# Kernel optimization log

Measured on AMD Instinct MI355X. Metric: run time of the kernel, lower is better.

The kernel has to match this reference:

```python
import jax, jax.numpy as jnp
import numpy as np

IMG = 1024.0          # input image size (square)
PRE_NMS_TOPK = 1000   # per level (test-time)
POST_NMS_TOPK = 1000
NMS_THRESH = 0.7
MIN_BOX_SIZE = 0.0
A = 3                 # anchors (aspect ratios) per location
SIZES = [32, 64, 128, 256, 512]
STRIDES = [4, 8, 16, 32, 64]
FEATS = [256, 128, 64, 32, 16]
RATIOS = [0.5, 1.0, 2.0]
B = 8


def _make_anchors():
    out = []
    for size, stride, f in zip(SIZES, STRIDES, FEATS):
        base = np.stack([np.array([-size * np.sqrt(r) / 2, -size / np.sqrt(r) / 2,
                                   size * np.sqrt(r) / 2, size / np.sqrt(r) / 2])
                         for r in RATIOS])  # [A,4]
        c = (np.arange(f) + 0.5) * stride
        cx, cy = np.meshgrid(c, c)
        shifts = np.stack([cx.ravel(), cy.ravel(), cx.ravel(), cy.ravel()], 1)  # [f*f,4]
        anc = (shifts[:, None, :] + base[None, :, :]).reshape(-1, 4)  # [f*f*A,4]
        out.append(anc.astype(np.float32))
    return out


def setup_inputs() -> dict:
    key = jax.random.key(0)
    ancs = _make_anchors()
    inp = {}
    for i, (lvl, anc) in enumerate(zip(["p2", "p3", "p4", "p5", "p6"], ancs)):
        n = anc.shape[0]
        kd, kc = jax.random.split(jax.random.fold_in(key, i))
        # Box2BoxTransformLinear deltas: (l,t,r,b) distances normalized by anchor size
        inp[f"deltas_{lvl}"] = jax.random.uniform(kd, (B, n, 4), jnp.float32, 0.05, 0.6)
        inp[f"ctr_{lvl}"] = jax.random.normal(kc, (B, n), jnp.float32)
        inp[f"anchors_{lvl}"] = jnp.asarray(anc)
    return inp


def _decode_linear(deltas, anchors):
    # Box2BoxTransformLinear(normalize_by_size=True).apply_deltas
    x1, y1, x2, y2 = anchors[..., 0], anchors[..., 1], anchors[..., 2], anchors[..., 3]
    w, h = x2 - x1, y2 - y1
    cx, cy = (x1 + x2) * 0.5, (y1 + y2) * 0.5
    dl, dt, dr, db = deltas[..., 0], deltas[..., 1], deltas[..., 2], deltas[..., 3]
    return jnp.stack([cx - dl * w, cy - dt * h, cx + dr * w, cy + db * h], -1)


def _iou_matrix(b):
    area = jnp.clip(b[:, 2] - b[:, 0], 0.0) * jnp.clip(b[:, 3] - b[:, 1], 0.0)
    lt = jnp.maximum(b[:, None, :2], b[None, :, :2])
    rb = jnp.minimum(b[:, None, 2:], b[None, :, 2:])
    wh = jnp.clip(rb - lt, 0.0)
    inter = wh[..., 0] * wh[..., 1]
    return inter / (area[:, None] + area[None, :] - inter + 1e-8)


def _nms_one(args):
    boxes_off, boxes, scores = args  # [N,4],[N,4],[N]
    order = jnp.argsort(-scores)
    bo, b, s = boxes_off[order], boxes[order], scores[order]
    iou = _iou_matrix(jax.lax.stop_gradient(bo))  # keep mask is non-differentiable
    n = s.shape[0]
    idxs = jnp.arange(n)
    keep0 = s > -jnp.inf

    def body(i, keep):
        sup = (iou[i] > NMS_THRESH) & (idxs > i) & keep[i]
        return keep & (~sup)

    keep = jax.lax.fori_loop(0, n, body, keep0)
    s_keep = jnp.where(keep, s, -jnp.inf)
    top_s, top_i = jax.lax.top_k(s_keep, POST_NMS_TOPK)
    return b[top_i], top_s


def _forward(deltas_list, ctr_list, anchors_list):
    boxes_all, scores_all, lvl_all = [], [], []
    for li, (d, c, a) in enumerate(zip(deltas_list, ctr_list, anchors_list)):
        boxes = _decode_linear(d, a)               # [B,Ni,4]
        k = min(PRE_NMS_TOPK, c.shape[1])
        s_top, idx = jax.lax.top_k(c, k)           # per-image per-level topk
        boxes_top = jnp.take_along_axis(boxes, idx[:, :, None], axis=1)
        boxes_all.append(boxes_top)
        scores_all.append(s_top)
        lvl_all.append(jnp.full((k,), float(li), jnp.float32))
    boxes = jnp.concatenate(boxes_all, axis=1)     # [B,N,4]
    scores = jnp.concatenate(scores_all, axis=1)   # [B,N]
    lvl = jnp.concatenate(lvl_all)                 # [N]

    boxes = jnp.clip(boxes, 0.0, IMG)              # clip to image
    w = boxes[..., 2] - boxes[..., 0]
    h = boxes[..., 3] - boxes[..., 1]
    valid = (w > MIN_BOX_SIZE) & (h > MIN_BOX_SIZE)
    scores = jnp.where(valid, scores, -jnp.inf)
    # batched (per-level) NMS via coordinate offsets
    boxes_off = boxes + lvl[None, :, None] * (IMG + 1.0)

    out_boxes, out_scores = jax.lax.map(_nms_one, (boxes_off, boxes, scores))
    return jnp.concatenate([out_boxes, out_scores[..., None]], -1)  # [B,POST,5]


def reference(deltas_p2, deltas_p3, deltas_p4, deltas_p5, deltas_p6,
              ctr_p2, ctr_p3, ctr_p4, ctr_p5, ctr_p6,
              anchors_p2, anchors_p3, anchors_p4, anchors_p5, anchors_p6):
    return _forward([deltas_p2, deltas_p3, deltas_p4, deltas_p5, deltas_p6],
                    [ctr_p2, ctr_p3, ctr_p4, ctr_p5, ctr_p6],
                    [anchors_p2, anchors_p3, anchors_p4, anchors_p5, anchors_p6])
```

## Files before the change

### kernel.cpp

```cpp
#include <hip/hip_runtime.h>
#include <cstdint>
#include <cstddef>
#include <cmath>

#pragma clang fp contract(off)

namespace {

constexpr int kCandMax = 4096;

__device__ __constant__ int c_N[5] = {196608, 49152, 12288, 3072, 768};
__device__ __constant__ int c_K[5] = {1000, 1000, 1000, 1000, 768};

struct RPNParams {
  const float* deltas[5];
  const float* ctr[5];
  const float* anchors[5];
  float* scores;
  float* boxes;
  unsigned char* keep;
  unsigned int* mask;
  unsigned int* g0p;
  unsigned int* g1p;
  unsigned int* ccount;
  unsigned int* v0kk;
  unsigned long long* cand;
  unsigned long long* keyC;
  float* out;
};

__device__ __forceinline__ unsigned int fkey(float f) {
  unsigned int u = __float_as_uint(f);
  return (u & 0x80000000u) ? ~u : (u | 0x80000000u);
}

__device__ __forceinline__ unsigned long long readlane64(unsigned long long v, int lane) {
  unsigned int lo = __builtin_amdgcn_readlane((unsigned int)v, lane);
  unsigned int hi = __builtin_amdgcn_readlane((unsigned int)(v >> 32), lane);
  return ((unsigned long long)hi << 32) | (unsigned long long)lo;
}

__global__ __launch_bounds__(256) void k_hist0(RPNParams P) {
  int bl = blockIdx.x, b = bl / 5, l = bl % 5;
  int N = c_N[l];
  int chunk = (N + 31) / 32;
  int i0 = blockIdx.y * chunk;
  int i1 = i0 + chunk; if (i1 > N) i1 = N;
  const float4* c4 = (const float4*)(P.ctr[l] + (size_t)b * N);
  __shared__ unsigned int wh[4][256];
  int tid = threadIdx.x, wid = tid >> 6;
  if (blockIdx.y == 0 && tid == 0) P.ccount[bl * 256] = 0u;
  for (int i = tid; i < 1024; i += 256) ((unsigned int*)wh)[i] = 0u;
  __syncthreads();
  int q0 = i0 >> 2, q1 = i1 >> 2;
  for (int q = q0 + tid; q < q1; q += 256) {
    float4 v = c4[q];
    atomicAdd(&wh[wid][fkey(v.x) >> 24], 1u);
    atomicAdd(&wh[wid][fkey(v.y) >> 24], 1u);
    atomicAdd(&wh[wid][fkey(v.z) >> 24], 1u);
    atomicAdd(&wh[wid][fkey(v.w) >> 24], 1u);
  }
  __syncthreads();
  int bin = tid;
  P.g0p[((size_t)bl * 32 + blockIdx.y) * 256 + bin] =
      wh[0][bin] + wh[1][bin] + wh[2][bin] + wh[3][bin];
}

__global__ __launch_bounds__(256) void k_hist1(RPNParams P) {
  int bl = blockIdx.x, b = bl / 5, l = bl % 5;
  int N = c_N[l], K = c_K[l];
  int chunk = (N + 31) / 32;
  int i0 = blockIdx.y * chunk;
  int i1 = i0 + chunk; if (i1 > N) i1 = N;
  const float4* c4 = (const float4*)(P.ctr[l] + (size_t)b * N);
  __shared__ unsigned int S[257];
  __shared__ unsigned int wh[4][256];
  int tid = threadIdx.x, wid = tid >> 6;
  {
    unsigned int s = 0;
    const unsigned int* base0 = P.g0p + (size_t)bl * 32 * 256 + tid;
    #pragma unroll 8
    for (int p = 0; p < 32; ++p) s += base0[p * 256];
    S[tid] = s;
    if (tid == 0) S[256] = 0u;
  }
  __syncthreads();
  for (int d = 1; d < 256; d <<= 1) {
    unsigned int v = (tid + d < 256) ? S[tid + d] : 0u;
    __syncthreads();
    S[tid] += v;
    __syncthreads();
  }
  int lo = 0, hi = 255;
  while (lo < hi) { int mid = (lo + hi + 1) >> 1; if (S[mid] >= (unsigned int)K) lo = mid; else hi = mid - 1; }
  unsigned int v0 = (unsigned int)lo;
  if (blockIdx.y == 0 && tid == 0) {
    P.v0kk[bl * 2] = v0;
    P.v0kk[bl * 2 + 1] = (unsigned int)K - S[lo + 1];
  }
  for (int i = tid; i < 1024; i += 256) ((unsigned int*)wh)[i] = 0u;
  __syncthreads();
  int q0 = i0 >> 2, q1 = i1 >> 2;
  for (int q = q0 + tid; q < q1; q += 256) {
    float4 v = c4[q];
    unsigned int u0 = fkey(v.x), u1 = fkey(v.y), u2 = fkey(v.z), u3 = fkey(v.w);
    if ((u0 >> 24) == v0) atomicAdd(&wh[wid][(u0 >> 16) & 255u], 1u);
    if ((u1 >> 24) == v0) atomicAdd(&wh[wid][(u1 >> 16) & 255u], 1u);
    if ((u2 >> 24) == v0) atomicAdd(&wh[wid][(u2 >> 16) & 255u], 1u);
    if ((u3 >> 24) == v0) atomicAdd(&wh[wid][(u3 >> 16) & 255u], 1u);
  }
  __syncthreads();
  int bin = tid;
  P.g1p[((size_t)bl * 32 + blockIdx.y) * 256 + bin] =
      wh[0][bin] + wh[1][bin] + wh[2][bin] + wh[3][bin];
}

__global__ __launch_bounds__(256) void k_compact(RPNParams P) {
  int bl = blockIdx.x, b = bl / 5, l = bl % 5;
  int N = c_N[l];
  int chunk = (N + 31) / 32;
  int i0 = blockIdx.y * chunk;
  int i1 = i0 + chunk; if (i1 > N) i1 = N;
  const float4* c4 = (const float4*)(P.ctr[l] + (size_t)b * N);
  unsigned long long* cand = P.cand + (size_t)bl * kCandMax;
  __shared__ unsigned int S[257];
  __shared__ unsigned int wcnt[4], wbase[4];
  int tid = threadIdx.x, lane = tid & 63, wid = tid >> 6;
  {
    unsigned int s = 0;
    const unsigned int* base1 = P.g1p + (size_t)bl * 32 * 256 + tid;
    #pragma unroll 8
    for (int p = 0; p < 32; ++p) s += base1[p * 256];
    S[tid] = s;
    if (tid == 0) S[256] = 0u;
  }
  __syncthreads();
  for (int d = 1; d < 256; d <<= 1) {
    unsigned int v = (tid + d < 256) ? S[tid + d] : 0u;
    __syncthreads();
    S[tid] += v;
    __syncthreads();
  }
  unsigned int v0 = P.v0kk[bl * 2], kk = P.v0kk[bl * 2 + 1];
  int lo = 0, hi = 255;
  while (lo < hi) { int mid = (lo + hi + 1) >> 1; if (S[mid] >= kk) lo = mid; else hi = mid - 1; }
  unsigned int T = ((v0 << 8) | (unsigned int)lo) << 16;
  int q0 = i0 >> 2, q1 = i1 >> 2;
  unsigned int cnt = 0;
  for (int q = q0 + tid; q < q1; q += 256) {
    float4 v = c4[q];
    cnt += (fkey(v.x) >= T) + (fkey(v.y) >= T) + (fkey(v.z) >= T) + (fkey(v.w) >= T);
  }
  for (int d = 32; d > 0; d >>= 1) cnt += (unsigned int)__shfl_xor((int)cnt, d, 64);
  if (lane == 0) wcnt[wid] = cnt;
  __syncthreads();
  if (tid == 0) {
    unsigned int tot = wcnt[0] + wcnt[1] + wcnt[2] + wcnt[3];
    unsigned int base = tot ? atomicAdd(&P.ccount[bl * 256], tot) : 0u;
    unsigned int acc = base;
    for (int w = 0; w < 4; ++w) { unsigned int x = wcnt[w]; wbase[w] = acc; acc += x; }
  }
  __syncthreads();
  unsigned int off = wbase[wid];
  unsigned long long lmlt = (1ull << lane) - 1ull;
  for (int q = q0 + tid; q < q1; q += 256) {
    float4 v = c4[q];
    unsigned int u[4] = {fkey(v.x), fkey(v.y), fkey(v.z), fkey(v.w)};
    #pragma unroll
    for (int k = 0; k < 4; ++k) {
      bool pred = (u[k] >= T);
      unsigned long long m = __ballot(pred);
      if (pred) {
        unsigned int pos = off + (unsigned int)__popcll(m & lmlt);
        if (pos < (unsigned int)kCandMax) {
          unsigned int idx = (unsigned int)(q * 4 + k);
          cand[pos] = ((unsigned long long)u[k] << 32) |
                      (unsigned long long)(0xFFFFFFFFu - idx);
        }
      }
      off += (unsigned int)__popcll(m);
    }
  }
}

__global__ __launch_bounds__(1024) void k_select(RPNParams P) {
  int bl = blockIdx.x, b = bl / 5, l = bl % 5;
  int N = c_N[l], K = c_K[l];
  const float* ctr = P.ctr[l] + (size_t)b * N;
  __shared__ unsigned long long cand[kCandMax];
  __shared__ unsigned int wsum[16];
  __shared__ unsigned int sTot;
  int tid = threadIdx.x;
  int lane = tid & 63, wid = tid >> 6;
  int cc = (int)P.ccount[bl * 256]; if (cc > kCandMax) cc = kCandMax;
  const unsigned long long* gc = P.cand + (size_t)bl * kCandMax;
  for (int i = tid; i < cc; i += 1024) cand[i] = gc[i];
  int n2 = 1; while (n2 < cc) n2 <<= 1;
  for (int i = cc + tid; i < n2; i += 1024) cand[i] = 0ull;
  __syncthreads();
  for (int size = 2; size <= n2; size <<= 1) {
    for (int stride = size >> 1; stride > 0; stride >>= 1) {
      for (int i = tid; i < n2; i += 1024) {
        int j = i ^ stride;
        if (j > i) {
          unsigned long long a = cand[i], c2 = cand[j];
          bool sw = ((i & size) == 0) ? (a < c2) : (a > c2);
          if (sw) { cand[i] = c2; cand[j] = a; }
        }
      }
      __syncthreads();
    }
  }
  size_t sbase = ((size_t)b * 5 + l) * 1024;
  int r = tid;
  unsigned long long kc = 0ull;
  bool flag = false;
  if (r < K) {
    unsigned long long cv = cand[r];
    unsigned int idx = 0xFFFFFFFFu - (unsigned int)(cv & 0xFFFFFFFFu);
    float s = ctr[idx];
    float4 anc = *(const float4*)(P.anchors[l] + (size_t)idx * 4);
    float4 dd  = *(const float4*)(P.deltas[l] + ((size_t)b * N + idx) * 4);
    float w = anc.z - anc.x, hgt = anc.w - anc.y;
    float cx = (anc.x + anc.z) * 0.5f, cy = (anc.y + anc.w) * 0.5f;
    float x1 = cx - dd.x * w;
    float y1 = cy - dd.y * hgt;
    float x2 = cx + dd.z * w;
    float y2 = cy + dd.w * hgt;
    x1 = fminf(fmaxf(x1, 0.0f), 1024.0f);
    y1 = fminf(fmaxf(y1, 0.0f), 1024.0f);
    x2 = fminf(fmaxf(x2, 0.0f), 1024.0f);
    y2 = fminf(fmaxf(y2, 0.0f), 1024.0f);
    bool valid = ((x2 - x1) > 0.0f) && ((y2 - y1) > 0.0f);
    float sc = valid ? s : -INFINITY;
    P.scores[sbase + r] = sc;
    *(float4*)(P.boxes + (sbase + r) * 4) = make_float4(x1, y1, x2, y2);
    unsigned int fk = fkey(sc);
    flag = fk > 0x007FFFFFu;
    unsigned int cidx = (unsigned int)(l * 1000 + r);
    kc = ((unsigned long long)fk << 32) |
         (unsigned long long)(0xFFFFFFFFu - cidx);
  }
  unsigned int fv = flag ? 1u : 0u, v = fv;
  for (int d = 1; d < 64; d <<= 1) {
    unsigned int n = __shfl_up(v, (unsigned int)d, 64);
    if (lane >= d) v += n;
  }
  if (lane == 63) wsum[wid] = v;
  __syncthreads();
  if (tid == 0) {
    unsigned int acc = 0;
    for (int w = 0; w < 16; ++w) { unsigned int x = wsum[w]; wsum[w] = acc; acc += x; }
    sTot = acc;
  }
  __syncthreads();
  unsigned int excl = wsum[wid] + (v - fv);
  if (r < K) {
    unsigned int dest = flag ? excl : (sTot + ((unsigned int)r - excl));
    P.keyC[(size_t)bl * 1024 + dest] = kc;
  }
}

__global__ __launch_bounds__(512) void k_mask(RPNParams P) {
  int bl = blockIdx.x, b = bl / 5, l = bl % 5;
  int K = c_K[l];
  int tid = threadIdx.x;
  int lane = tid & 63;
  int yg = blockIdx.y * 8 + (tid >> 6);
  int zc = blockIdx.z;
  float off = (float)l * 1025.0f;
  size_t sbase = ((size_t)b * 5 + l) * 1024;
  __shared__ alignas(16) float4 obox[1024];
  __shared__ float area[1024];
  for (int i = tid; i < 1024; i += 512) {
    float4 v = make_float4(0.f, 0.f, 0.f, 0.f);
    if (i < K) {
      v = ((const float4*)P.boxes)[sbase + i];
      v.x += off; v.y += off; v.z += off; v.w += off;
    }
    obox[i] = v;
    area[i] = fmaxf(v.z - v.x, 0.0f) * fmaxf(v.w - v.y, 0.0f);
  }
  __syncthreads();
  int i = yg * 64 + lane;
  if (i >= K) return;
  float4 bi = obox[i];
  float ai = area[i];
  unsigned int* mrow = P.mask + (sbase + (size_t)i) * 32;
  const double M = 0x1.666667p-1;
  auto pr = [&](int j) -> bool {
    float4 bj = obox[j];
    float aj = area[j];
    float xx1 = fmaxf(bi.x, bj.x);
    float yy1 = fmaxf(bi.y, bj.y);
    float xx2 = fminf(bi.z, bj.z);
    float yy2 = fminf(bi.w, bj.w);
    float ww = fmaxf(xx2 - xx1, 0.0f);
    float hh = fmaxf(yy2 - yy1, 0.0f);
    float inter = ww * hh;
    float uni = ai + aj - inter + 1e-8f;
    return (double)inter >= M * (double)uni;
  };
  int wown = 2 * yg;
  if (zc == 0) {
    for (int w = 0; w < wown; ++w) mrow[w] = 0u;
    unsigned int m0, m1;
    if (lane < 32) { m0 = (1u << lane) - 1u; m1 = 0u; }
    else           { m0 = 0xFFFFFFFFu; m1 = (1u << (lane - 32)) - 1u; }
    #pragma unroll
    for (int h = 0; h < 2; ++h) {
      unsigned int bits = 0u;
      int j0 = (wown + h) << 5;
      for (int jj = 0; jj < 32; ++jj)
        if (pr(j0 + jj)) bits |= (1u << jj);
      mrow[wown + h] = bits & (h ? m1 : m0);
    }
  }
  int wstart = wown + 2;
  int nw = 32 - wstart;
  int qlen = (nw + 15) >> 4;
  int wbeg = wstart + zc * qlen;
  int wend = wbeg + qlen; if (wend > 32) wend = 32;
  for (int w = wbeg; w < wend; ++w) {
    unsigned int bits = 0u;
    int j0 = w << 5;
    for (int jj = 0; jj < 32; ++jj)
      if (pr(j0 + jj)) bits |= (1u << jj);
    mrow[w] = bits;
  }
}

__global__ __launch_bounds__(1024) void k_sweep(RPNParams P) {
  int bl = blockIdx.x, b = bl / 5, l = bl % 5;
  int K = c_K[l];
  int NW = (K + 63) >> 6;
  size_t sbase = ((size_t)b * 5 + l) * 1024;
  __shared__ alignas(16) unsigned long long lmask[16 * 1000];
  __shared__ unsigned long long rdiag[1024];
  __shared__ unsigned long long svalid[16];
  __shared__ unsigned long long skept[16];
  int tid = threadIdx.x;
  const ulonglong2* gm2 = (const ulonglong2*)(P.mask + sbase * 32);
  for (int j = tid; j < K * 8; j += 1024) {
    ulonglong2 v = gm2[j];
    ((ulonglong2*)lmask)[j] = v;
    int w0i = j * 2;
    int row = w0i >> 4;
    int dcol = row >> 6;
    int col0 = w0i & 15;
    if (col0 == dcol) rdiag[row] = v.x;
    else if (col0 + 1 == dcol) rdiag[row] = v.y;
  }
  {
    int g = tid >> 6;
    int e = g * 64 + (tid & 63);
    bool pred = (e < K) && (P.scores[sbase + e] > -INFINITY);
    unsigned long long m = __ballot(pred);
    if ((tid & 63) == 0) svalid[g] = m;
  }
  __syncthreads();
  if (tid >= 64) return;
  int lane = tid;
  int sub = lane >> 4, col = lane & 15;
  unsigned long long accA = 0ull, accB = 0ull;
  for (int g = 0; g < NW; ++g) {
    unsigned long long am = accA | accB;
    unsigned long long suppr = readlane64(am, g) | readlane64(am, g + 16) |
                               readlane64(am, g + 32) | readlane64(am, g + 48);
    unsigned long long A = svalid[g] & ~suppr;
    unsigned long long colmask = rdiag[g * 64 + lane];
    unsigned long long kept = 0ull;
    while (A) {
      bool cand = (A >> lane) & 1ull;
      unsigned long long D = __ballot(cand && ((colmask & A) == 0ull));
      kept |= D;
      unsigned long long sup = __ballot((colmask & D) != 0ull);
      A &= ~(D | sup);
    }
    if (lane == 0) skept[g] = kept;
    const unsigned long long* rowbase = &lmask[((size_t)g * 64 + (size_t)sub) * 16 + col];
    #pragma unroll
    for (int t = 0; t < 8; ++t) {
      int p0 = (2 * t) * 4 + sub;
      int p1 = (2 * t + 1) * 4 + sub;
      unsigned long long s0 = 0ull - ((kept >> p0) & 1ull);
      unsigned long long s1 = 0ull - ((kept >> p1) & 1ull);
      accA |= rowbase[(size_t)(2 * t) * 64] & s0;
      accB |= rowbase[(size_t)(2 * t + 1) * 64] & s1;
    }
  }
  for (int g = 0; g < NW; ++g) {
    unsigned long long kv = skept[g];
    int e = g * 64 + lane;
    if (e < K) P.keep[sbase + e] = (unsigned char)((kv >> lane) & 1ull);
  }
}

__global__ __launch_bounds__(1024) void k_merge(RPNParams P) {
  int b = blockIdx.x;
  __shared__ unsigned long long keyL[5][1000];
  __shared__ unsigned short srt[4768];
  __shared__ unsigned int wsum[16];
  __shared__ unsigned int sTot;
  int tid = threadIdx.x;
  int lane = tid & 63, wid = tid >> 6;

  #pragma unroll
  for (int l = 0; l < 5; ++l)
    if (tid < c_K[l]) keyL[l][tid] = P.keyC[((size_t)b * 5 + l) * 1024 + tid];
  __syncthreads();

  for (int e = tid; e < 4768; e += 1024) {
    int l = (e < 4000) ? (e / 1000) : 4;
    int p = e - l * 1000;
    unsigned long long k = keyL[l][p];
    int rank = p;
    #pragma unroll
    for (int l2 = 0; l2 < 5; ++l2) {
      if (l2 == l) continue;
      int lo = 0, hi = c_K[l2];
      while (lo < hi) {
        int mid = (lo + hi) >> 1;
        if (keyL[l2][mid] > k) lo = mid + 1; else hi = mid;
      }
      rank += lo;
    }
    srt[rank] = (unsigned short)(0xFFFFFFFFu - (unsigned int)(k & 0xFFFFFFFFu));
  }
  __syncthreads();

  int base = tid * 5;
  unsigned char lf[5];
  unsigned short lc[5];
  unsigned int lsum = 0;
  for (int q = 0; q < 5; ++q) {
    int i = base + q;
    unsigned char f = 0; unsigned short cx = 0;
    if (i < 4768) {
      cx = srt[i];
      int l = cx / 1000;
      int r = (int)cx - l * 1000;
      f = P.keep[((size_t)b * 5 + l) * 1024 + r];
    }
    lf[q] = f; lc[q] = cx; lsum += f;
  }
  unsigned int v = lsum;
  for (int d = 1; d < 64; d <<= 1) {
    unsigned int n = __shfl_up(v, (unsigned int)d, 64);
    if (lane >= d) v += n;
  }
  if (lane == 63) wsum[wid] = v;
  __syncthreads();
  if (tid == 0) {
    unsigned int acc = 0;
    for (int w = 0; w < 16; ++w) { unsigned int x = wsum[w]; wsum[w] = acc; acc += x; }
    sTot = acc;
  }
  __syncthreads();
  unsigned int excl = wsum[wid] + (v - lsum);
  unsigned int tot = sTot;
  for (int q = 0; q < 5; ++q) {
    int i = base + q;
    if (i >= 4768) break;
    unsigned int cidx = (unsigned int)lc[q];
    int l = (int)(cidx / 1000u);
    int r = (int)cidx - l * 1000;
    size_t sb = ((size_t)b * 5 + l) * 1024 + r;
    unsigned char f = lf[q];
    unsigned int pos = f ? excl : (tot + ((unsigned int)i - excl));
    excl += f;
    if (pos < 1000u) {
      float4 bx = ((const float4*)P.boxes)[sb];
      float sc = f ? P.scores[sb] : -INFINITY;
      float* o = P.out + ((size_t)b * 1000 + pos) * 5;
      o[0] = bx.x; o[1] = bx.y; o[2] = bx.z; o[3] = bx.w; o[4] = sc;
    }
  }
}

}

extern "C" void kernel_launch(void* const* d_in, const int* in_sizes, int n_in,
                              void* d_out, int out_size, void* d_ws, size_t ws_size,
                              hipStream_t stream) {
  (void)out_size; (void)ws_size;
  RPNParams P;
  bool interleaved = (n_in >= 3) && (in_sizes[2] == 786432);
  for (int l = 0; l < 5; ++l) {
    if (interleaved) {
      P.deltas[l]  = (const float*)d_in[3 * l + 0];
      P.ctr[l]     = (const float*)d_in[3 * l + 1];
      P.anchors[l] = (const float*)d_in[3 * l + 2];
    } else {
      P.deltas[l]  = (const float*)d_in[l];
      P.ctr[l]     = (const float*)d_in[5 + l];
      P.anchors[l] = (const float*)d_in[10 + l];
    }
  }
  char* ws = (char*)d_ws;
  P.scores = (float*)(ws + 0);
  P.boxes  = (float*)(ws + 163840);
  P.keep   = (unsigned char*)(ws + 819200);
  P.mask   = (unsigned int*)(ws + 860160);
  P.cand   = (unsigned long long*)(ws + 860160);
  P.g0p    = (unsigned int*)(ws + 2170880);
  P.g1p    = (unsigned int*)(ws + 3481600);
  P.ccount = (unsigned int*)(ws + 6103040);
  P.v0kk   = (unsigned int*)(ws + 6144000);
  P.keyC   = (unsigned long long*)(ws + 6144320);
  P.out    = (float*)d_out;

  hipLaunchKernelGGL(k_hist0, dim3(40, 32), dim3(256), 0, stream, P);
  hipLaunchKernelGGL(k_hist1, dim3(40, 32), dim3(256), 0, stream, P);
  hipLaunchKernelGGL(k_compact, dim3(40, 32), dim3(256), 0, stream, P);
  hipLaunchKernelGGL(k_select, dim3(40), dim3(1024), 0, stream, P);
  hipLaunchKernelGGL(k_mask, dim3(40, 2, 16), dim3(512), 0, stream, P);
  hipLaunchKernelGGL(k_sweep, dim3(40), dim3(1024), 0, stream, P);
  hipLaunchKernelGGL(k_merge, dim3(8), dim3(1024), 0, stream, P);
}
```

Baseline: 113.4 us.

## Fuse histogram and compaction passes into one cooperative kernel with grid sync

Merges the three top-k selection passes (coarse histogram, fine histogram, compaction) into a single cooperative launch separated by grid-wide barriers. The aim is to remove two kernel launch gaps and let the ctr data stay warm in cache between passes. It also splits the first-pass shared histogram into 16 sub-histograms per block to reduce LDS atomic contention. If the cooperative launch fails it falls back to the three separate kernels. Grid sync has its own cost, and the larger shared-memory struct may reduce occupancy, though 1280 blocks of 256 threads should still fit co-resident.

New measurement: 413.9 us. 3.65x slower.

```diff
diff --git a/kernel.cpp b/kernel.cpp
--- a/kernel.cpp
+++ b/kernel.cpp
@@ -1,9 +1,12 @@
 #include <hip/hip_runtime.h>
+#include <hip/hip_cooperative_groups.h>
 #include <cstdint>
 #include <cstddef>
 #include <cmath>
 
 #pragma clang fp contract(off)
+
+namespace cg = cooperative_groups;
 
 namespace {
 
@@ -40,110 +43,121 @@
   return ((unsigned long long)hi << 32) | (unsigned long long)lo;
 }
 
-__global__ __launch_bounds__(256) void k_hist0(RPNParams P) {
-  int bl = blockIdx.x, b = bl / 5, l = bl % 5;
+struct Phase1Smem {
+  unsigned int wh16[4][4][257];
+  unsigned int wh1[4][256];
+  unsigned int S[257];
+  unsigned int wcnt[4], wbase[4];
+};
+
+__device__ __forceinline__ void phaseA_hist0(const RPNParams& P, Phase1Smem& sm,
+                                             int bl, int y) {
+  int b = bl / 5, l = bl % 5;
   int N = c_N[l];
   int chunk = (N + 31) / 32;
-  int i0 = blockIdx.y * chunk;
+  int i0 = y * chunk;
   int i1 = i0 + chunk; if (i1 > N) i1 = N;
   const float4* c4 = (const float4*)(P.ctr[l] + (size_t)b * N);
-  __shared__ unsigned int wh[4][256];
-  int tid = threadIdx.x, wid = tid >> 6;
-  if (blockIdx.y == 0 && tid == 0) P.ccount[bl * 256] = 0u;
-  for (int i = tid; i < 1024; i += 256) ((unsigned int*)wh)[i] = 0u;
-  __syncthreads();
+  int tid = threadIdx.x, wid = tid >> 6, sg = tid & 3;
+  if (y == 0 && tid == 0) P.ccount[bl * 256] = 0u;
+  for (int i = tid; i < 4 * 4 * 257; i += 256) ((unsigned int*)sm.wh16)[i] = 0u;
+  __syncthreads();
+  unsigned int* myh = sm.wh16[wid][sg];
   int q0 = i0 >> 2, q1 = i1 >> 2;
   for (int q = q0 + tid; q < q1; q += 256) {
     float4 v = c4[q];
-    atomicAdd(&wh[wid][fkey(v.x) >> 24], 1u);
-    atomicAdd(&wh[wid][fkey(v.y) >> 24], 1u);
-    atomicAdd(&wh[wid][fkey(v.z) >> 24], 1u);
-    atomicAdd(&wh[wid][fkey(v.w) >> 24], 1u);
+    atomicAdd(&myh[fkey(v.x) >> 24], 1u);
+    atomicAdd(&myh[fkey(v.y) >> 24], 1u);
+    atomicAdd(&myh[fkey(v.z) >> 24], 1u);
+    atomicAdd(&myh[fkey(v.w) >> 24], 1u);
   }
   __syncthreads();
   int bin = tid;
-  P.g0p[((size_t)bl * 32 + blockIdx.y) * 256 + bin] =
-      wh[0][bin] + wh[1][bin] + wh[2][bin] + wh[3][bin];
-}
-
-__global__ __launch_bounds__(256) void k_hist1(RPNParams P) {
-  int bl = blockIdx.x, b = bl / 5, l = bl % 5;
+  unsigned int s = 0;
+  #pragma unroll
+  for (int w = 0; w < 4; ++w)
+    #pragma unroll
+    for (int k2 = 0; k2 < 4; ++k2) s += sm.wh16[w][k2][bin];
+  P.g0p[((size_t)bl * 32 + y) * 256 + bin] = s;
+}
+
+__device__ __forceinline__ void phaseB_hist1(const RPNParams& P, Phase1Smem& sm,
+                                             int bl, int y) {
+  int b = bl / 5, l = bl % 5;
   int N = c_N[l], K = c_K[l];
   int chunk = (N + 31) / 32;
-  int i0 = blockIdx.y * chunk;
+  int i0 = y * chunk;
   int i1 = i0 + chunk; if (i1 > N) i1 = N;
   const float4* c4 = (const float4*)(P.ctr[l] + (size_t)b * N);
-  __shared__ unsigned int S[257];
-  __shared__ unsigned int wh[4][256];
   int tid = threadIdx.x, wid = tid >> 6;
   {
     unsigned int s = 0;
     const unsigned int* base0 = P.g0p + (size_t)bl * 32 * 256 + tid;
     #pragma unroll 8
     for (int p = 0; p < 32; ++p) s += base0[p * 256];
-    S[tid] = s;
-    if (tid == 0) S[256] = 0u;
+    sm.S[tid] = s;
+    if (tid == 0) sm.S[256] = 0u;
   }
   __syncthreads();
   for (int d = 1; d < 256; d <<= 1) {
-    unsigned int v = (tid + d < 256) ? S[tid + d] : 0u;
+    unsigned int v = (tid + d < 256) ? sm.S[tid + d] : 0u;
     __syncthreads();
-    S[tid] += v;
+    sm.S[tid] += v;
     __syncthreads();
   }
   int lo = 0, hi = 255;
-  while (lo < hi) { int mid = (lo + hi + 1) >> 1; if (S[mid] >= (unsigned int)K) lo = mid; else hi = mid - 1; }
+  while (lo < hi) { int mid = (lo + hi + 1) >> 1; if (sm.S[mid] >= (unsigned int)K) lo = mid; else hi = mid - 1; }
   unsigned int v0 = (unsigned int)lo;
-  if (blockIdx.y == 0 && tid == 0) {
+  if (y == 0 && tid == 0) {
     P.v0kk[bl * 2] = v0;
-    P.v0kk[bl * 2 + 1] = (unsigned int)K - S[lo + 1];
-  }
-  for (int i = tid; i < 1024; i += 256) ((unsigned int*)wh)[i] = 0u;
+    P.v0kk[bl * 2 + 1] = (unsigned int)K - sm.S[lo + 1];
+  }
+  for (int i = tid; i < 1024; i += 256) ((unsigned int*)sm.wh1)[i] = 0u;
   __syncthreads();
   int q0 = i0 >> 2, q1 = i1 >> 2;
   for (int q = q0 + tid; q < q1; q += 256) {
     float4 v = c4[q];
     unsigned int u0 = fkey(v.x), u1 = fkey(v.y), u2 = fkey(v.z), u3 = fkey(v.w);
-    if ((u0 >> 24) == v0) atomicAdd(&wh[wid][(u0 >> 16) & 255u], 1u);
-    if ((u1 >> 24) == v0) atomicAdd(&wh[wid][(u1 >> 16) & 255u], 1u);
-    if ((u2 >> 24) == v0) atomicAdd(&wh[wid][(u2 >> 16) & 255u], 1u);
-    if ((u3 >> 24) == v0) atomicAdd(&wh[wid][(u3 >> 16) & 255u], 1u);
+    if ((u0 >> 24) == v0) atomicAdd(&sm.wh1[wid][(u0 >> 16) & 255u], 1u);
+    if ((u1 >> 24) == v0) atomicAdd(&sm.wh1[wid][(u1 >> 16) & 255u], 1u);
+    if ((u2 >> 24) == v0) atomicAdd(&sm.wh1[wid][(u2 >> 16) & 255u], 1u);
+    if ((u3 >> 24) == v0) atomicAdd(&sm.wh1[wid][(u3 >> 16) & 255u], 1u);
   }
   __syncthreads();
   int bin = tid;
-  P.g1p[((size_t)bl * 32 + blockIdx.y) * 256 + bin] =
-      wh[0][bin] + wh[1][bin] + wh[2][bin] + wh[3][bin];
-}
-
-__global__ __launch_bounds__(256) void k_compact(RPNParams P) {
-  int bl = blockIdx.x, b = bl / 5, l = bl % 5;
+  P.g1p[((size_t)bl * 32 + y) * 256 + bin] =
+      sm.wh1[0][bin] + sm.wh1[1][bin] + sm.wh1[2][bin] + sm.wh1[3][bin];
+}
+
+__device__ __forceinline__ void phaseC_compact(const RPNParams& P, Phase1Smem& sm,
+                                               int bl, int y) {
+  int b = bl / 5, l = bl % 5;
   int N = c_N[l];
   int chunk = (N + 31) / 32;
-  int i0 = blockIdx.y * chunk;
+  int i0 = y * chunk;
   int i1 = i0 + chunk; if (i1 > N) i1 = N;
   const float4* c4 = (const float4*)(P.ctr[l] + (size_t)b * N);
   unsigned long long* cand = P.cand + (size_t)bl * kCandMax;
-  __shared__ unsigned int S[257];
-  __shared__ unsigned int wcnt[4], wbase[4];
   int tid = threadIdx.x, lane = tid & 63, wid = tid >> 6;
+  __syncthreads();
   {
     unsigned int s = 0;
     const unsigned int* base1 = P.g1p + (size_t)bl * 32 * 256 + tid;
     #pragma unroll 8
     for (int p = 0; p < 32; ++p) s += base1[p * 256];
-    S[tid] = s;
-    if (tid == 0) S[256] = 0u;
+    sm.S[tid] = s;
+    if (tid == 0) sm.S[256] = 0u;
   }
   __syncthreads();
   for (int d = 1; d < 256; d <<= 1) {
-    unsigned int v = (tid + d < 256) ? S[tid + d] : 0u;
+    unsigned int v = (tid + d < 256) ? sm.S[tid + d] : 0u;
     __syncthreads();
-    S[tid] += v;
+    sm.S[tid] += v;
     __syncthreads();
   }
   unsigned int v0 = P.v0kk[bl * 2], kk = P.v0kk[bl * 2 + 1];
   int lo = 0, hi = 255;
-  while (lo < hi) { int mid = (lo + hi + 1) >> 1; if (S[mid] >= kk) lo = mid; else hi = mid - 1; }
+  while (lo < hi) { int mid = (lo + hi + 1) >> 1; if (sm.S[mid] >= kk) lo = mid; else hi = mid - 1; }
   unsigned int T = ((v0 << 8) | (unsigned int)lo) << 16;
   int q0 = i0 >> 2, q1 = i1 >> 2;
   unsigned int cnt = 0;
@@ -152,16 +166,16 @@
     cnt += (fkey(v.x) >= T) + (fkey(v.y) >= T) + (fkey(v.z) >= T) + (fkey(v.w) >= T);
   }
   for (int d = 32; d > 0; d >>= 1) cnt += (unsigned int)__shfl_xor((int)cnt, d, 64);
-  if (lane == 0) wcnt[wid] = cnt;
+  if (lane == 0) sm.wcnt[wid] = cnt;
   __syncthreads();
   if (tid == 0) {
-    unsigned int tot = wcnt[0] + wcnt[1] + wcnt[2] + wcnt[3];
+    unsigned int tot = sm.wcnt[0] + sm.wcnt[1] + sm.wcnt[2] + sm.wcnt[3];
     unsigned int base = tot ? atomicAdd(&P.ccount[bl * 256], tot) : 0u;
     unsigned int acc = base;
-    for (int w = 0; w < 4; ++w) { unsigned int x = wcnt[w]; wbase[w] = acc; acc += x; }
-  }
-  __syncthreads();
-  unsigned int off = wbase[wid];
+    for (int w = 0; w < 4; ++w) { unsigned int x = sm.wcnt[w]; sm.wbase[w] = acc; acc += x; }
+  }
+  __syncthreads();
+  unsigned int off = sm.wbase[wid];
   unsigned long long lmlt = (1ull << lane) - 1ull;
   for (int q = q0 + tid; q < q1; q += 256) {
     float4 v = c4[q];
@@ -181,6 +195,30 @@
       off += (unsigned int)__popcll(m);
     }
   }
+}
+
+__global__ __launch_bounds__(256) void k_phase1(RPNParams P) {
+  __shared__ Phase1Smem sm;
+  cg::grid_group grid = cg::this_grid();
+  int bl = blockIdx.x, y = blockIdx.y;
+  phaseA_hist0(P, sm, bl, y);
+  grid.sync();
+  phaseB_hist1(P, sm, bl, y);
+  grid.sync();
+  phaseC_compact(P, sm, bl, y);
+}
+
+__global__ __launch_bounds__(256) void k_hist0(RPNParams P) {
+  __shared__ Phase1Smem sm;
+  phaseA_hist0(P, sm, blockIdx.x, blockIdx.y);
+}
+__global__ __launch_bounds__(256) void k_hist1(RPNParams P) {
+  __shared__ Phase1Smem sm;
+  phaseB_hist1(P, sm, blockIdx.x, blockIdx.y);
+}
+__global__ __launch_bounds__(256) void k_compact(RPNParams P) {
+  __shared__ Phase1Smem sm;
+  phaseC_compact(P, sm, blockIdx.x, blockIdx.y);
 }
 
 __global__ __launch_bounds__(1024) void k_select(RPNParams P) {
@@ -510,9 +548,15 @@
   P.keyC   = (unsigned long long*)(ws + 6144320);
   P.out    = (float*)d_out;
 
-  hipLaunchKernelGGL(k_hist0, dim3(40, 32), dim3(256), 0, stream, P);
-  hipLaunchKernelGGL(k_hist1, dim3(40, 32), dim3(256), 0, stream, P);
-  hipLaunchKernelGGL(k_compact, dim3(40, 32), dim3(256), 0, stream, P);
+  void* kargs[] = { (void*)&P };
+  hipError_t ce = hipLaunchCooperativeKernel((const void*)k_phase1,
+                                             dim3(40, 32), dim3(256),
+                                             kargs, 0, stream);
+  if (ce != hipSuccess) {
+    hipLaunchKernelGGL(k_hist0, dim3(40, 32), dim3(256), 0, stream, P);
+    hipLaunchKernelGGL(k_hist1, dim3(40, 32), dim3(256), 0, stream, P);
+    hipLaunchKernelGGL(k_compact, dim3(40, 32), dim3(256), 0, stream, P);
+  }
   hipLaunchKernelGGL(k_select, dim3(40), dim3(1024), 0, stream, P);
   hipLaunchKernelGGL(k_mask, dim3(40, 2, 16), dim3(512), 0, stream, P);
   hipLaunchKernelGGL(k_sweep, dim3(40), dim3(1024), 0, stream, P);
```

## Fuse candidate compaction into select kernel and privatize hist0 sub-histograms

Applied to the files above, without the earlier changes.

Removes the separate k_compact launch and its global candidate buffer and counter. Each k_select block now rescans its whole level and appends candidates straight into shared memory, using a per-wavefront LDS atomic counter. k_hist0 also spreads its atomics over 16 private sub-histograms per block (padded to 257) to cut LDS atomic contention. The trade-off is that compaction now runs on only 40 blocks, each streaming a full level, instead of 1280 blocks.

Result: slower. 128.5 us (+13.3%).

```diff
diff --git a/kernel.cpp b/kernel.cpp
--- a/kernel.cpp
+++ b/kernel.cpp
@@ -22,9 +22,7 @@
   unsigned int* mask;
   unsigned int* g0p;
   unsigned int* g1p;
-  unsigned int* ccount;
   unsigned int* v0kk;
-  unsigned long long* cand;
   unsigned long long* keyC;
   float* out;
 };
@@ -47,23 +45,27 @@
   int i0 = blockIdx.y * chunk;
   int i1 = i0 + chunk; if (i1 > N) i1 = N;
   const float4* c4 = (const float4*)(P.ctr[l] + (size_t)b * N);
-  __shared__ unsigned int wh[4][256];
-  int tid = threadIdx.x, wid = tid >> 6;
-  if (blockIdx.y == 0 && tid == 0) P.ccount[bl * 256] = 0u;
-  for (int i = tid; i < 1024; i += 256) ((unsigned int*)wh)[i] = 0u;
-  __syncthreads();
+  __shared__ unsigned int wh16[4][4][257];
+  int tid = threadIdx.x, wid = tid >> 6, sg = tid & 3;
+  for (int i = tid; i < 4 * 4 * 257; i += 256) ((unsigned int*)wh16)[i] = 0u;
+  __syncthreads();
+  unsigned int* myh = wh16[wid][sg];
   int q0 = i0 >> 2, q1 = i1 >> 2;
   for (int q = q0 + tid; q < q1; q += 256) {
     float4 v = c4[q];
-    atomicAdd(&wh[wid][fkey(v.x) >> 24], 1u);
-    atomicAdd(&wh[wid][fkey(v.y) >> 24], 1u);
-    atomicAdd(&wh[wid][fkey(v.z) >> 24], 1u);
-    atomicAdd(&wh[wid][fkey(v.w) >> 24], 1u);
+    atomicAdd(&myh[fkey(v.x) >> 24], 1u);
+    atomicAdd(&myh[fkey(v.y) >> 24], 1u);
+    atomicAdd(&myh[fkey(v.z) >> 24], 1u);
+    atomicAdd(&myh[fkey(v.w) >> 24], 1u);
   }
   __syncthreads();
   int bin = tid;
-  P.g0p[((size_t)bl * 32 + blockIdx.y) * 256 + bin] =
-      wh[0][bin] + wh[1][bin] + wh[2][bin] + wh[3][bin];
+  unsigned int s = 0;
+  #pragma unroll
+  for (int w = 0; w < 4; ++w)
+    #pragma unroll
+    for (int k2 = 0; k2 < 4; ++k2) s += wh16[w][k2][bin];
+  P.g0p[((size_t)bl * 32 + blockIdx.y) * 256 + bin] = s;
 }
 
 __global__ __launch_bounds__(256) void k_hist1(RPNParams P) {
@@ -115,86 +117,71 @@
       wh[0][bin] + wh[1][bin] + wh[2][bin] + wh[3][bin];
 }
 
-__global__ __launch_bounds__(256) void k_compact(RPNParams P) {
+__global__ __launch_bounds__(1024) void k_select(RPNParams P) {
   int bl = blockIdx.x, b = bl / 5, l = bl % 5;
-  int N = c_N[l];
-  int chunk = (N + 31) / 32;
-  int i0 = blockIdx.y * chunk;
-  int i1 = i0 + chunk; if (i1 > N) i1 = N;
-  const float4* c4 = (const float4*)(P.ctr[l] + (size_t)b * N);
-  unsigned long long* cand = P.cand + (size_t)bl * kCandMax;
+  int N = c_N[l], K = c_K[l];
+  const float* ctr = P.ctr[l] + (size_t)b * N;
+  const float4* c4 = (const float4*)ctr;
+  __shared__ unsigned long long cand[kCandMax];
+  __shared__ unsigned int S4[4][256];
   __shared__ unsigned int S[257];
-  __shared__ unsigned int wcnt[4], wbase[4];
-  int tid = threadIdx.x, lane = tid & 63, wid = tid >> 6;
+  __shared__ unsigned int candCount;
+  __shared__ unsigned int wsum[16];
+  __shared__ unsigned int sTot;
+  int tid = threadIdx.x;
+  int lane = tid & 63, wid = tid >> 6;
   {
+    int bin = tid & 255, qq = tid >> 8;
     unsigned int s = 0;
-    const unsigned int* base1 = P.g1p + (size_t)bl * 32 * 256 + tid;
-    #pragma unroll 8
-    for (int p = 0; p < 32; ++p) s += base1[p * 256];
-    S[tid] = s;
+    const unsigned int* base1 = P.g1p + (size_t)bl * 32 * 256 + bin;
+    #pragma unroll
+    for (int p = 0; p < 8; ++p) s += base1[(qq * 8 + p) * 256];
+    S4[qq][bin] = s;
+  }
+  if (tid == 0) candCount = 0u;
+  __syncthreads();
+  if (tid < 256) {
+    S[tid] = S4[0][tid] + S4[1][tid] + S4[2][tid] + S4[3][tid];
     if (tid == 0) S[256] = 0u;
   }
   __syncthreads();
   for (int d = 1; d < 256; d <<= 1) {
-    unsigned int v = (tid + d < 256) ? S[tid + d] : 0u;
+    unsigned int v = 0;
+    if (tid < 256 && tid + d < 256) v = S[tid + d];
     __syncthreads();
-    S[tid] += v;
+    if (tid < 256) S[tid] += v;
     __syncthreads();
   }
   unsigned int v0 = P.v0kk[bl * 2], kk = P.v0kk[bl * 2 + 1];
   int lo = 0, hi = 255;
   while (lo < hi) { int mid = (lo + hi + 1) >> 1; if (S[mid] >= kk) lo = mid; else hi = mid - 1; }
   unsigned int T = ((v0 << 8) | (unsigned int)lo) << 16;
-  int q0 = i0 >> 2, q1 = i1 >> 2;
-  unsigned int cnt = 0;
-  for (int q = q0 + tid; q < q1; q += 256) {
-    float4 v = c4[q];
-    cnt += (fkey(v.x) >= T) + (fkey(v.y) >= T) + (fkey(v.z) >= T) + (fkey(v.w) >= T);
-  }
-  for (int d = 32; d > 0; d >>= 1) cnt += (unsigned int)__shfl_xor((int)cnt, d, 64);
-  if (lane == 0) wcnt[wid] = cnt;
-  __syncthreads();
-  if (tid == 0) {
-    unsigned int tot = wcnt[0] + wcnt[1] + wcnt[2] + wcnt[3];
-    unsigned int base = tot ? atomicAdd(&P.ccount[bl * 256], tot) : 0u;
-    unsigned int acc = base;
-    for (int w = 0; w < 4; ++w) { unsigned int x = wcnt[w]; wbase[w] = acc; acc += x; }
-  }
-  __syncthreads();
-  unsigned int off = wbase[wid];
+  int qn = N >> 2;
   unsigned long long lmlt = (1ull << lane) - 1ull;
-  for (int q = q0 + tid; q < q1; q += 256) {
+  for (int q = tid; q < qn; q += 1024) {
     float4 v = c4[q];
     unsigned int u[4] = {fkey(v.x), fkey(v.y), fkey(v.z), fkey(v.w)};
     #pragma unroll
     for (int k = 0; k < 4; ++k) {
       bool pred = (u[k] >= T);
       unsigned long long m = __ballot(pred);
-      if (pred) {
-        unsigned int pos = off + (unsigned int)__popcll(m & lmlt);
-        if (pos < (unsigned int)kCandMax) {
-          unsigned int idx = (unsigned int)(q * 4 + k);
-          cand[pos] = ((unsigned long long)u[k] << 32) |
-                      (unsigned long long)(0xFFFFFFFFu - idx);
+      if (m) {
+        unsigned int base = 0;
+        if (lane == 0) base = atomicAdd(&candCount, (unsigned int)__popcll(m));
+        base = (unsigned int)__shfl((int)base, 0, 64);
+        if (pred) {
+          unsigned int pos = base + (unsigned int)__popcll(m & lmlt);
+          if (pos < (unsigned int)kCandMax) {
+            unsigned int idx = (unsigned int)(q * 4 + k);
+            cand[pos] = ((unsigned long long)u[k] << 32) |
+                        (unsigned long long)(0xFFFFFFFFu - idx);
+          }
         }
       }
-      off += (unsigned int)__popcll(m);
-    }
-  }
-}
-
-__global__ __launch_bounds__(1024) void k_select(RPNParams P) {
-  int bl = blockIdx.x, b = bl / 5, l = bl % 5;
-  int N = c_N[l], K = c_K[l];
-  const float* ctr = P.ctr[l] + (size_t)b * N;
-  __shared__ unsigned long long cand[kCandMax];
-  __shared__ unsigned int wsum[16];
-  __shared__ unsigned int sTot;
-  int tid = threadIdx.x;
-  int lane = tid & 63, wid = tid >> 6;
-  int cc = (int)P.ccount[bl * 256]; if (cc > kCandMax) cc = kCandMax;
-  const unsigned long long* gc = P.cand + (size_t)bl * kCandMax;
-  for (int i = tid; i < cc; i += 1024) cand[i] = gc[i];
+    }
+  }
+  __syncthreads();
+  int cc = (int)candCount; if (cc > kCandMax) cc = kCandMax;
   int n2 = 1; while (n2 < cc) n2 <<= 1;
   for (int i = cc + tid; i < n2; i += 1024) cand[i] = 0ull;
   __syncthreads();
@@ -502,17 +489,14 @@
   P.boxes  = (float*)(ws + 163840);
   P.keep   = (unsigned char*)(ws + 819200);
   P.mask   = (unsigned int*)(ws + 860160);
-  P.cand   = (unsigned long long*)(ws + 860160);
   P.g0p    = (unsigned int*)(ws + 2170880);
   P.g1p    = (unsigned int*)(ws + 3481600);
-  P.ccount = (unsigned int*)(ws + 6103040);
   P.v0kk   = (unsigned int*)(ws + 6144000);
   P.keyC   = (unsigned long long*)(ws + 6144320);
   P.out    = (float*)d_out;
 
   hipLaunchKernelGGL(k_hist0, dim3(40, 32), dim3(256), 0, stream, P);
   hipLaunchKernelGGL(k_hist1, dim3(40, 32), dim3(256), 0, stream, P);
-  hipLaunchKernelGGL(k_compact, dim3(40, 32), dim3(256), 0, stream, P);
   hipLaunchKernelGGL(k_select, dim3(40), dim3(1024), 0, stream, P);
   hipLaunchKernelGGL(k_mask, dim3(40, 2, 16), dim3(512), 0, stream, P);
   hipLaunchKernelGGL(k_sweep, dim3(40), dim3(1024), 0, stream, P);
```

## Replace two-pass radix top-k threshold with single 12-bit histogram pass

Applied to the files above, without the earlier changes.

Merges the two radix-histogram kernels (8-bit then 8-bit refinement) into one kernel that builds a 4096-bin histogram on the top 12 key bits, stored as 16-bit partial counts. The compact kernel now derives the threshold directly from that histogram with a per-thread 16-bin suffix sum and an atomicMax. This removes one full pass over the scores and one launch, at the cost of a coarser threshold that lets more candidates past compaction, which could overflow the candidate buffer or add work to later selection. Chunk sizes now assume N divides evenly by 8 and 32.

After: 116.2 us. 2.4% more time.

```diff
diff --git a/kernel.cpp b/kernel.cpp
--- a/kernel.cpp
+++ b/kernel.cpp
@@ -20,10 +20,8 @@
   float* boxes;
   unsigned char* keep;
   unsigned int* mask;
-  unsigned int* g0p;
-  unsigned int* g1p;
+  unsigned short* g12;
   unsigned int* ccount;
-  unsigned int* v0kk;
   unsigned long long* cand;
   unsigned long long* keyC;
   float* out;
@@ -40,48 +38,59 @@
   return ((unsigned long long)hi << 32) | (unsigned long long)lo;
 }
 
-__global__ __launch_bounds__(256) void k_hist0(RPNParams P) {
+__global__ __launch_bounds__(512) void k_hist(RPNParams P) {
   int bl = blockIdx.x, b = bl / 5, l = bl % 5;
   int N = c_N[l];
-  int chunk = (N + 31) / 32;
+  int chunk = N / 8;
   int i0 = blockIdx.y * chunk;
-  int i1 = i0 + chunk; if (i1 > N) i1 = N;
   const float4* c4 = (const float4*)(P.ctr[l] + (size_t)b * N);
-  __shared__ unsigned int wh[4][256];
-  int tid = threadIdx.x, wid = tid >> 6;
+  __shared__ unsigned int wh[4][4096];
+  int tid = threadIdx.x;
+  int cp = tid >> 7;
   if (blockIdx.y == 0 && tid == 0) P.ccount[bl * 256] = 0u;
-  for (int i = tid; i < 1024; i += 256) ((unsigned int*)wh)[i] = 0u;
-  __syncthreads();
-  int q0 = i0 >> 2, q1 = i1 >> 2;
-  for (int q = q0 + tid; q < q1; q += 256) {
+  for (int i = tid; i < 4096; i += 512) ((uint4*)wh)[i] = make_uint4(0, 0, 0, 0);
+  __syncthreads();
+  unsigned int* myh = wh[cp];
+  int q0 = i0 >> 2, q1 = (i0 + chunk) >> 2;
+  for (int q = q0 + tid; q < q1; q += 512) {
     float4 v = c4[q];
-    atomicAdd(&wh[wid][fkey(v.x) >> 24], 1u);
-    atomicAdd(&wh[wid][fkey(v.y) >> 24], 1u);
-    atomicAdd(&wh[wid][fkey(v.z) >> 24], 1u);
-    atomicAdd(&wh[wid][fkey(v.w) >> 24], 1u);
-  }
-  __syncthreads();
-  int bin = tid;
-  P.g0p[((size_t)bl * 32 + blockIdx.y) * 256 + bin] =
-      wh[0][bin] + wh[1][bin] + wh[2][bin] + wh[3][bin];
-}
-
-__global__ __launch_bounds__(256) void k_hist1(RPNParams P) {
+    atomicAdd(&myh[fkey(v.x) >> 20], 1u);
+    atomicAdd(&myh[fkey(v.y) >> 20], 1u);
+    atomicAdd(&myh[fkey(v.z) >> 20], 1u);
+    atomicAdd(&myh[fkey(v.w) >> 20], 1u);
+  }
+  __syncthreads();
+  unsigned short* dst = P.g12 + ((size_t)bl * 8 + blockIdx.y) * 4096;
+  for (int bin = tid; bin < 4096; bin += 512)
+    dst[bin] = (unsigned short)(wh[0][bin] + wh[1][bin] + wh[2][bin] + wh[3][bin]);
+}
+
+__global__ __launch_bounds__(256) void k_compact(RPNParams P) {
   int bl = blockIdx.x, b = bl / 5, l = bl % 5;
-  int N = c_N[l], K = c_K[l];
-  int chunk = (N + 31) / 32;
+  int N = c_N[l];
+  unsigned int K = (unsigned int)c_K[l];
+  int chunk = N / 32;
   int i0 = blockIdx.y * chunk;
-  int i1 = i0 + chunk; if (i1 > N) i1 = N;
   const float4* c4 = (const float4*)(P.ctr[l] + (size_t)b * N);
+  unsigned long long* cand = P.cand + (size_t)bl * kCandMax;
   __shared__ unsigned int S[257];
-  __shared__ unsigned int wh[4][256];
-  int tid = threadIdx.x, wid = tid >> 6;
+  __shared__ int sV;
+  __shared__ unsigned int wcnt[4], wbase[4];
+  int tid = threadIdx.x, lane = tid & 63, wid = tid >> 6;
+  if (tid == 0) sV = 0;
+  unsigned int ls[16];
   {
-    unsigned int s = 0;
-    const unsigned int* base0 = P.g0p + (size_t)bl * 32 * 256 + tid;
-    #pragma unroll 8
-    for (int p = 0; p < 32; ++p) s += base0[p * 256];
-    S[tid] = s;
+    const unsigned short* base = P.g12 + (size_t)bl * 8 * 4096 + tid * 16;
+    #pragma unroll
+    for (int j = 0; j < 16; ++j) {
+      unsigned int s = 0;
+      #pragma unroll
+      for (int p = 0; p < 8; ++p) s += base[p * 4096 + j];
+      ls[j] = s;
+    }
+    #pragma unroll
+    for (int j = 14; j >= 0; --j) ls[j] += ls[j + 1];
+    S[tid] = ls[0];
     if (tid == 0) S[256] = 0u;
   }
   __syncthreads();
@@ -91,61 +100,17 @@
     S[tid] += v;
     __syncthreads();
   }
-  int lo = 0, hi = 255;
-  while (lo < hi) { int mid = (lo + hi + 1) >> 1; if (S[mid] >= (unsigned int)K) lo = mid; else hi = mid - 1; }
-  unsigned int v0 = (unsigned int)lo;
-  if (blockIdx.y == 0 && tid == 0) {
-    P.v0kk[bl * 2] = v0;
-    P.v0kk[bl * 2 + 1] = (unsigned int)K - S[lo + 1];
-  }
-  for (int i = tid; i < 1024; i += 256) ((unsigned int*)wh)[i] = 0u;
-  __syncthreads();
-  int q0 = i0 >> 2, q1 = i1 >> 2;
-  for (int q = q0 + tid; q < q1; q += 256) {
-    float4 v = c4[q];
-    unsigned int u0 = fkey(v.x), u1 = fkey(v.y), u2 = fkey(v.z), u3 = fkey(v.w);
-    if ((u0 >> 24) == v0) atomicAdd(&wh[wid][(u0 >> 16) & 255u], 1u);
-    if ((u1 >> 24) == v0) atomicAdd(&wh[wid][(u1 >> 16) & 255u], 1u);
-    if ((u2 >> 24) == v0) atomicAdd(&wh[wid][(u2 >> 16) & 255u], 1u);
-    if ((u3 >> 24) == v0) atomicAdd(&wh[wid][(u3 >> 16) & 255u], 1u);
-  }
-  __syncthreads();
-  int bin = tid;
-  P.g1p[((size_t)bl * 32 + blockIdx.y) * 256 + bin] =
-      wh[0][bin] + wh[1][bin] + wh[2][bin] + wh[3][bin];
-}
-
-__global__ __launch_bounds__(256) void k_compact(RPNParams P) {
-  int bl = blockIdx.x, b = bl / 5, l = bl % 5;
-  int N = c_N[l];
-  int chunk = (N + 31) / 32;
-  int i0 = blockIdx.y * chunk;
-  int i1 = i0 + chunk; if (i1 > N) i1 = N;
-  const float4* c4 = (const float4*)(P.ctr[l] + (size_t)b * N);
-  unsigned long long* cand = P.cand + (size_t)bl * kCandMax;
-  __shared__ unsigned int S[257];
-  __shared__ unsigned int wcnt[4], wbase[4];
-  int tid = threadIdx.x, lane = tid & 63, wid = tid >> 6;
   {
-    unsigned int s = 0;
-    const unsigned int* base1 = P.g1p + (size_t)bl * 32 * 256 + tid;
-    #pragma unroll 8
-    for (int p = 0; p < 32; ++p) s += base1[p * 256];
-    S[tid] = s;
-    if (tid == 0) S[256] = 0u;
-  }
-  __syncthreads();
-  for (int d = 1; d < 256; d <<= 1) {
-    unsigned int v = (tid + d < 256) ? S[tid + d] : 0u;
-    __syncthreads();
-    S[tid] += v;
-    __syncthreads();
-  }
-  unsigned int v0 = P.v0kk[bl * 2], kk = P.v0kk[bl * 2 + 1];
-  int lo = 0, hi = 255;
-  while (lo < hi) { int mid = (lo + hi + 1) >> 1; if (S[mid] >= kk) lo = mid; else hi = mid - 1; }
-  unsigned int T = ((v0 << 8) | (unsigned int)lo) << 16;
-  int q0 = i0 >> 2, q1 = i1 >> 2;
+    unsigned int excl = (tid < 255) ? S[tid + 1] : 0u;
+    int v = -1;
+    #pragma unroll
+    for (int j = 15; j >= 0; --j)
+      if (v < 0 && ls[j] + excl >= K) v = tid * 16 + j;
+    if (v >= 0) atomicMax(&sV, v);
+  }
+  __syncthreads();
+  unsigned int T = ((unsigned int)sV) << 20;
+  int q0 = i0 >> 2, q1 = (i0 + chunk) >> 2;
   unsigned int cnt = 0;
   for (int q = q0 + tid; q < q1; q += 256) {
     float4 v = c4[q];
@@ -503,15 +468,12 @@
   P.keep   = (unsigned char*)(ws + 819200);
   P.mask   = (unsigned int*)(ws + 860160);
   P.cand   = (unsigned long long*)(ws + 860160);
-  P.g0p    = (unsigned int*)(ws + 2170880);
-  P.g1p    = (unsigned int*)(ws + 3481600);
+  P.g12    = (unsigned short*)(ws + 2170880);
   P.ccount = (unsigned int*)(ws + 6103040);
-  P.v0kk   = (unsigned int*)(ws + 6144000);
   P.keyC   = (unsigned long long*)(ws + 6144320);
   P.out    = (float*)d_out;
 
-  hipLaunchKernelGGL(k_hist0, dim3(40, 32), dim3(256), 0, stream, P);
-  hipLaunchKernelGGL(k_hist1, dim3(40, 32), dim3(256), 0, stream, P);
+  hipLaunchKernelGGL(k_hist, dim3(40, 8), dim3(512), 0, stream, P);
   hipLaunchKernelGGL(k_compact, dim3(40, 32), dim3(256), 0, stream, P);
   hipLaunchKernelGGL(k_select, dim3(40), dim3(1024), 0, stream, P);
   hipLaunchKernelGGL(k_mask, dim3(40, 2, 16), dim3(512), 0, stream, P);
```
